# Kernel tuning notes

Measured on AMD Instinct MI355X. Metric: run time of the kernel, lower is better.

The kernel has to match this reference:

```python
import jax, jax.numpy as jnp
import numpy as np

N = 12288          # atoms
G = 12             # graphs in batch
R = 1536           # residues
K = 32             # max_num_neighbors
RADIUS = 5.0
MIN_DISTANCE = 5
EPS = 1e-10


def setup_inputs() -> dict:
    key = jax.random.key(0)
    k1, k2, k3 = jax.random.split(key, 3)
    # positions in a 50 A box -> protein-like density (~a few neighbors in r=5)
    node_position = jax.random.uniform(k1, (N, 3), dtype=jnp.float32) * 50.0
    node2graph = jnp.sort(jax.random.randint(k2, (N,), 0, G, dtype=jnp.int32))
    atom2residue = jnp.sort(jax.random.randint(k3, (N,), 0, R, dtype=jnp.int32))
    return {"node_position": node_position, "node2graph": node2graph,
            "atom2residue": atom2residue}


def _select_neighbors(node_position, node2graph):
    """For each node i, pick up to K nearest same-graph nodes within RADIUS.
    Returns idx [N,K] (neighbor indices) and in_radius [N,K] (validity)."""
    n = node_position.shape[0]
    sq = jnp.sum(node_position * node_position, axis=-1)            # [N]
    d2 = sq[:, None] + sq[None, :] - 2.0 * (node_position @ node_position.T)
    d2 = jnp.maximum(d2, 0.0)                                        # [N,N]
    ar = jnp.arange(n)
    valid = (node2graph[:, None] == node2graph[None, :]) \
            & (ar[:, None] != ar[None, :]) \
            & (d2 <= RADIUS * RADIUS)
    nd2 = jnp.where(valid, d2, jnp.inf)
    neg_d2, idx = jax.lax.top_k(-nd2, K)                             # nearest K
    in_radius = jnp.isfinite(neg_d2)
    return idx, in_radius


def reference(node_position, node2graph, atom2residue):
    n = node_position.shape[0]
    idx, in_radius = _select_neighbors(node_position, node2graph)
    node_out = jnp.repeat(jnp.arange(n, dtype=jnp.int32), K)         # center i
    node_in = idx.reshape(-1).astype(jnp.int32)                      # neighbor j
    valid = in_radius.reshape(-1)
    # residue-distance filter: drop |res_in - res_out| < min_distance
    res_diff = jnp.abs(atom2residue[node_in] - atom2residue[node_out])
    valid = valid & (res_diff >= MIN_DISTANCE)
    # drop near-coincident positions (||p_i - p_j|| < eps)
    diff = node_position[node_in] - node_position[node_out]
    d2_sel = jnp.sum(diff * diff, axis=-1)
    valid = valid & (d2_sel >= EPS * EPS)
    relation = jnp.zeros_like(node_in)
    edge_list = jnp.stack([node_in, node_out, relation], axis=-1)    # [N*K,3]
    edge_list = jnp.where(valid[:, None], edge_list, -1)             # pad invalid
    return edge_list, valid, jnp.int32(1)
```

## Files before the change

kernel.cpp:

```cpp
#include <hip/hip_runtime.h>

#define EDGE_K 32
#define CAP    256

__global__ __launch_bounds__(64) void spatial_edge_kernel(
    const float* __restrict__ pos,
    const int* __restrict__ n2g,
    const int* __restrict__ a2r,
    int* __restrict__ out,
    int n)
{
    const int i    = blockIdx.x;
    const int lane = threadIdx.x;

    __shared__ float sd2[CAP];
    __shared__ int   sj[CAP];
    __shared__ float rd2[EDGE_K];
    __shared__ int   rj[EDGE_K];

    const float xi = pos[3*i+0];
    const float yi = pos[3*i+1];
    const float zi = pos[3*i+2];
    const float si = xi*xi + yi*yi + zi*zi;
    const int g  = n2g[i];
    const int ri = a2r[i];

    int lo = 0, hi = n;
    while (lo < hi) { int m = (lo + hi) >> 1; if (n2g[m] < g) lo = m + 1; else hi = m; }
    const int jstart = lo;
    hi = n;
    while (lo < hi) { int m = (lo + hi) >> 1; if (n2g[m] <= g) lo = m + 1; else hi = m; }
    const int jend = lo;

    int count = 0;
    for (int j0 = jstart; j0 < jend; j0 += 64) {
        const int j = j0 + lane;
        bool pass = false;
        float d2 = 0.0f;
        if (j < jend && j != i) {
            const float xj = pos[3*j+0];
            const float yj = pos[3*j+1];
            const float zj = pos[3*j+2];
            const float sj2 = xj*xj + yj*yj + zj*zj;
            const float dt  = xi*xj + yi*yj + zi*zj;
            d2 = si + sj2 - 2.0f*dt;
            d2 = fmaxf(d2, 0.0f);
            pass = (d2 <= 25.0f);
        }
        const unsigned long long mask = __ballot(pass);
        if (pass) {
            const int idx = count + __popcll(mask & ((1ull << lane) - 1ull));
            if (idx < CAP) { sd2[idx] = d2; sj[idx] = j; }
        }
        count += __popcll(mask);
    }
    __syncthreads();

    int cnt;
    if (count <= CAP) {
        const int m = count;
        for (int c = lane; c < m; c += 64) {
            const float dc = sd2[c];
            const int   jc = sj[c];
            int rank = 0;
            for (int t = 0; t < m; ++t) {
                const float dt_ = sd2[t];
                const int   jt  = sj[t];
                rank += (dt_ < dc) || (dt_ == dc && jt < jc);
            }
            if (rank < EDGE_K) { rd2[rank] = dc; rj[rank] = jc; }
        }
        cnt = (m < EDGE_K) ? m : EDGE_K;
    } else {
        if (lane == 0) {
            float bd[EDGE_K];
            int   bj[EDGE_K];
            int c2 = 0;
            for (int j = jstart; j < jend; ++j) {
                if (j == i) continue;
                const float xj = pos[3*j+0];
                const float yj = pos[3*j+1];
                const float zj = pos[3*j+2];
                const float sj2 = xj*xj + yj*yj + zj*zj;
                const float dt  = xi*xj + yi*yj + zi*zj;
                float d2 = si + sj2 - 2.0f*dt;
                d2 = fmaxf(d2, 0.0f);
                if (d2 > 25.0f) continue;
                if (c2 == EDGE_K && d2 >= bd[EDGE_K-1]) continue;
                int p = (c2 < EDGE_K) ? c2 : (EDGE_K - 1);
                while (p > 0 && bd[p-1] > d2) {
                    bd[p] = bd[p-1]; bj[p] = bj[p-1]; --p;
                }
                bd[p] = d2; bj[p] = j;
                if (c2 < EDGE_K) ++c2;
            }
            for (int k = 0; k < c2; ++k) { rd2[k] = bd[k]; rj[k] = bj[k]; }
        }
        cnt = (count < EDGE_K) ? count : EDGE_K;
    }
    __syncthreads();

    const int NK = n * EDGE_K;
    int* valid_out = out + 3 * NK;
    if (lane < EDGE_K) {
        const int k = lane;
        int a = -1, b = -1, c = -1, v = 0;
        if (k < cnt) {
            const int j  = rj[k];
            const int rjres = a2r[j];
            const int rd = (rjres > ri) ? (rjres - ri) : (ri - rjres);
            const float dx = pos[3*j+0] - xi;
            const float dy = pos[3*j+1] - yi;
            const float dz = pos[3*j+2] - zi;
            const float d2s = dx*dx + dy*dy + dz*dz;
            if (rd >= 5 && d2s >= 1e-20f) { a = j; b = i; c = 0; v = 1; }
        }
        const int e = i * EDGE_K + k;
        out[3*e+0] = a;
        out[3*e+1] = b;
        out[3*e+2] = c;
        valid_out[e] = v;
    }
    if (i == 0 && lane == 0) out[4*NK] = 1;
}

extern "C" void kernel_launch(void* const* d_in, const int* in_sizes, int n_in,
                              void* d_out, int out_size, void* d_ws, size_t ws_size,
                              hipStream_t stream) {
    const float* pos = (const float*)d_in[0];
    const int*   n2g = (const int*)d_in[1];
    const int*   a2r = (const int*)d_in[2];
    int* out = (int*)d_out;
    const int n = in_sizes[0] / 3;
    hipLaunchKernelGGL(spatial_edge_kernel, dim3(n), dim3(64), 0, stream,
                       pos, n2g, a2r, out, n);
}
```

Before: 33.86 us.

## Pack positions into float4 and process four atoms per block

A pre-pass kernel copies positions into an aligned float4 workspace, so the inner distance scan issues one 16-byte load per neighbor instead of three strided scalar loads. The main kernel now runs four waves per block, one atom per wave. Candidate distance/index pairs are stored as int2 in shared memory, and the candidate cap is lowered to fit four waves. The extra launch and workspace write add overhead, and the packed path only runs when a large enough aligned workspace is provided.

```diff
diff --git a/kernel.cpp b/kernel.cpp
--- a/kernel.cpp
+++ b/kernel.cpp
@@ -1,36 +1,55 @@
 #include <hip/hip_runtime.h>
 
 #define EDGE_K 32
-#define CAP    256
+#define CAP    128
+#define WPB    4
 
-__global__ __launch_bounds__(64) void spatial_edge_kernel(
+__global__ __launch_bounds__(256) void pack_kernel(
+    const float* __restrict__ pos, float4* __restrict__ pk, int n)
+{
+    int i = blockIdx.x * blockDim.x + threadIdx.x;
+    if (i < n) {
+        pk[i] = make_float4(pos[3*i+0], pos[3*i+1], pos[3*i+2], 0.0f);
+    }
+}
+
+template<bool PACKED>
+__global__ __launch_bounds__(WPB * 64) void spatial_edge_kernel(
     const float* __restrict__ pos,
+    const float4* __restrict__ pk,
     const int* __restrict__ n2g,
     const int* __restrict__ a2r,
     int* __restrict__ out,
     int n)
 {
-    const int i    = blockIdx.x;
-    const int lane = threadIdx.x;
+    const int wave = threadIdx.x >> 6;
+    const int lane = threadIdx.x & 63;
+    const int i    = blockIdx.x * WPB + wave;
+    const bool active = (i < n);
 
-    __shared__ float sd2[CAP];
-    __shared__ int   sj[CAP];
-    __shared__ float rd2[EDGE_K];
-    __shared__ int   rj[EDGE_K];
+    __shared__ int2 scand[WPB][CAP];
+    __shared__ int2 sres[WPB][EDGE_K];
 
-    const float xi = pos[3*i+0];
-    const float yi = pos[3*i+1];
-    const float zi = pos[3*i+2];
-    const float si = xi*xi + yi*yi + zi*zi;
-    const int g  = n2g[i];
-    const int ri = a2r[i];
+    float xi = 0.f, yi = 0.f, zi = 0.f, si = 0.f;
+    int ri = 0, jstart = 0, jend = 0;
 
-    int lo = 0, hi = n;
-    while (lo < hi) { int m = (lo + hi) >> 1; if (n2g[m] < g) lo = m + 1; else hi = m; }
-    const int jstart = lo;
-    hi = n;
-    while (lo < hi) { int m = (lo + hi) >> 1; if (n2g[m] <= g) lo = m + 1; else hi = m; }
-    const int jend = lo;
+    if (active) {
+        if (PACKED) {
+            float4 p = pk[i];
+            xi = p.x; yi = p.y; zi = p.z;
+        } else {
+            xi = pos[3*i+0]; yi = pos[3*i+1]; zi = pos[3*i+2];
+        }
+        si = xi*xi + yi*yi + zi*zi;
+        const int g = n2g[i];
+        ri = a2r[i];
+        int lo = 0, hi = n;
+        while (lo < hi) { int m = (lo + hi) >> 1; if (n2g[m] < g) lo = m + 1; else hi = m; }
+        jstart = lo;
+        hi = n;
+        while (lo < hi) { int m = (lo + hi) >> 1; if (n2g[m] <= g) lo = m + 1; else hi = m; }
+        jend = lo;
+    }
 
     int count = 0;
     for (int j0 = jstart; j0 < jend; j0 += 64) {
@@ -38,9 +57,13 @@
         bool pass = false;
         float d2 = 0.0f;
         if (j < jend && j != i) {
-            const float xj = pos[3*j+0];
-            const float yj = pos[3*j+1];
-            const float zj = pos[3*j+2];
+            float xj, yj, zj;
+            if (PACKED) {
+                float4 p = pk[j];
+                xj = p.x; yj = p.y; zj = p.z;
+            } else {
+                xj = pos[3*j+0]; yj = pos[3*j+1]; zj = pos[3*j+2];
+            }
             const float sj2 = xj*xj + yj*yj + zj*zj;
             const float dt  = xi*xj + yi*yj + zi*zj;
             d2 = si + sj2 - 2.0f*dt;
@@ -49,38 +72,41 @@
         }
         const unsigned long long mask = __ballot(pass);
         if (pass) {
-            const int idx = count + __popcll(mask & ((1ull << lane) - 1ull));
-            if (idx < CAP) { sd2[idx] = d2; sj[idx] = j; }
+            const int idx = count +
+                (int)__builtin_amdgcn_mbcnt_hi((unsigned)(mask >> 32),
+                     __builtin_amdgcn_mbcnt_lo((unsigned)mask, 0u));
+            if (idx < CAP) scand[wave][idx] = make_int2(__float_as_int(d2), j);
         }
         count += __popcll(mask);
     }
     __syncthreads();
 
-    int cnt;
+    int cnt = 0;
     if (count <= CAP) {
         const int m = count;
         for (int c = lane; c < m; c += 64) {
-            const float dc = sd2[c];
-            const int   jc = sj[c];
+            const int2 e = scand[wave][c];
+            const float dc = __int_as_float(e.x);
+            const int   jc = e.y;
             int rank = 0;
             for (int t = 0; t < m; ++t) {
-                const float dt_ = sd2[t];
-                const int   jt  = sj[t];
-                rank += (dt_ < dc) || (dt_ == dc && jt < jc);
+                const int2 et = scand[wave][t];
+                const float dtv = __int_as_float(et.x);
+                rank += (dtv < dc) || (dtv == dc && et.y < jc);
             }
-            if (rank < EDGE_K) { rd2[rank] = dc; rj[rank] = jc; }
+            if (rank < EDGE_K) sres[wave][rank] = e;
         }
         cnt = (m < EDGE_K) ? m : EDGE_K;
-    } else {
+    } else if (active) {
         if (lane == 0) {
             float bd[EDGE_K];
             int   bj[EDGE_K];
             int c2 = 0;
             for (int j = jstart; j < jend; ++j) {
                 if (j == i) continue;
-                const float xj = pos[3*j+0];
-                const float yj = pos[3*j+1];
-                const float zj = pos[3*j+2];
+                float xj, yj, zj;
+                if (PACKED) { float4 p = pk[j]; xj = p.x; yj = p.y; zj = p.z; }
+                else { xj = pos[3*j+0]; yj = pos[3*j+1]; zj = pos[3*j+2]; }
                 const float sj2 = xj*xj + yj*yj + zj*zj;
                 const float dt  = xi*xj + yi*yj + zi*zj;
                 float d2 = si + sj2 - 2.0f*dt;
@@ -94,7 +120,8 @@
                 bd[p] = d2; bj[p] = j;
                 if (c2 < EDGE_K) ++c2;
             }
-            for (int k = 0; k < c2; ++k) { rd2[k] = bd[k]; rj[k] = bj[k]; }
+            for (int k = 0; k < c2; ++k)
+                sres[wave][k] = make_int2(__float_as_int(bd[k]), bj[k]);
         }
         cnt = (count < EDGE_K) ? count : EDGE_K;
     }
@@ -102,16 +129,19 @@
 
     const int NK = n * EDGE_K;
     int* valid_out = out + 3 * NK;
-    if (lane < EDGE_K) {
+    if (active && lane < EDGE_K) {
         const int k = lane;
         int a = -1, b = -1, c = -1, v = 0;
         if (k < cnt) {
-            const int j  = rj[k];
+            const int j = sres[wave][k].y;
             const int rjres = a2r[j];
             const int rd = (rjres > ri) ? (rjres - ri) : (ri - rjres);
-            const float dx = pos[3*j+0] - xi;
-            const float dy = pos[3*j+1] - yi;
-            const float dz = pos[3*j+2] - zi;
+            float xj, yj, zj;
+            if (PACKED) { float4 p = pk[j]; xj = p.x; yj = p.y; zj = p.z; }
+            else { xj = pos[3*j+0]; yj = pos[3*j+1]; zj = pos[3*j+2]; }
+            const float dx = xj - xi;
+            const float dy = yj - yi;
+            const float dz = zj - zi;
             const float d2s = dx*dx + dy*dy + dz*dz;
             if (rd >= 5 && d2s >= 1e-20f) { a = j; b = i; c = 0; v = 1; }
         }
@@ -121,7 +151,7 @@
         out[3*e+2] = c;
         valid_out[e] = v;
     }
-    if (i == 0 && lane == 0) out[4*NK] = 1;
+    if (blockIdx.x == 0 && threadIdx.x == 0) out[4*NK] = 1;
 }
 
 extern "C" void kernel_launch(void* const* d_in, const int* in_sizes, int n_in,
@@ -132,6 +162,16 @@
     const int*   a2r = (const int*)d_in[2];
     int* out = (int*)d_out;
     const int n = in_sizes[0] / 3;
-    hipLaunchKernelGGL(spatial_edge_kernel, dim3(n), dim3(64), 0, stream,
-                       pos, n2g, a2r, out, n);
+    const int grid = (n + WPB - 1) / WPB;
+    const bool packed = (ws_size >= (size_t)n * sizeof(float4)) && (((uintptr_t)d_ws & 15) == 0);
+    if (packed) {
+        float4* pk = (float4*)d_ws;
+        hipLaunchKernelGGL(pack_kernel, dim3((n + 255) / 256), dim3(256), 0, stream,
+                           pos, pk, n);
+        hipLaunchKernelGGL(spatial_edge_kernel<true>, dim3(grid), dim3(WPB * 64), 0, stream,
+                           pos, (const float4*)pk, n2g, a2r, out, n);
+    } else {
+        hipLaunchKernelGGL(spatial_edge_kernel<false>, dim3(grid), dim3(WPB * 64), 0, stream,
+                           pos, (const float4*)nullptr, n2g, a2r, out, n);
+    }
 }
```

Measured after the change: 73.52 us. 117% more time.

## Add pre-pass packing positions to float4 and precomputing graph bounds

Applied to the files above, without the earlier changes.

A new pre-pass kernel packs positions into float4 in the workspace and computes per-graph start/end offsets, so the main kernel skips its two binary searches and does one vector load per neighbor. The neighbor scan is unrolled four chunks at a time to overlap loads, candidates are stored as int2 pairs, and the candidate buffer cap drops from 256 to 128. This adds a second launch and a fallback to the old kernel when the workspace is too small or misaligned. The smaller cap sends more atoms to the serial single-lane path if neighbor counts exceed 128.

```diff
diff --git a/kernel.cpp b/kernel.cpp
--- a/kernel.cpp
+++ b/kernel.cpp
@@ -1,100 +1,127 @@
 #include <hip/hip_runtime.h>
 
 #define EDGE_K 32
-#define CAP    256
-
-__global__ __launch_bounds__(64) void spatial_edge_kernel(
-    const float* __restrict__ pos,
+#define CAP    128
+#define NB     64
+
+__global__ __launch_bounds__(256) void pack_kernel(
+    const float* __restrict__ pos, const int* __restrict__ n2g,
+    float4* __restrict__ pk, int* __restrict__ bounds, int n)
+{
+    int i = blockIdx.x * blockDim.x + threadIdx.x;
+    if (i >= n) return;
+    pk[i] = make_float4(pos[3*i+0], pos[3*i+1], pos[3*i+2], 0.0f);
+    const int gi = n2g[i];
+    if (i == 0) {
+        for (int g = 0; g <= gi && g < NB; ++g) bounds[g] = 0;
+    } else {
+        const int gp = n2g[i-1];
+        if (gp != gi) for (int g = gp + 1; g <= gi && g < NB; ++g) bounds[g] = i;
+    }
+    if (i == n - 1) {
+        for (int g = gi + 1; g < NB; ++g) bounds[g] = n;
+    }
+}
+
+__global__ __launch_bounds__(64) void spatial_edge_fast(
+    const float4* __restrict__ pk,
     const int* __restrict__ n2g,
     const int* __restrict__ a2r,
-    int* __restrict__ out,
-    int n)
+    const int* __restrict__ bounds,
+    int* __restrict__ out, int n)
 {
     const int i    = blockIdx.x;
     const int lane = threadIdx.x;
 
-    __shared__ float sd2[CAP];
-    __shared__ int   sj[CAP];
-    __shared__ float rd2[EDGE_K];
-    __shared__ int   rj[EDGE_K];
-
-    const float xi = pos[3*i+0];
-    const float yi = pos[3*i+1];
-    const float zi = pos[3*i+2];
+    __shared__ int2 scand[CAP];
+    __shared__ int2 sres[EDGE_K];
+
+    const float4 pi = pk[i];
+    const float xi = pi.x, yi = pi.y, zi = pi.z;
     const float si = xi*xi + yi*yi + zi*zi;
     const int g  = n2g[i];
     const int ri = a2r[i];
 
-    int lo = 0, hi = n;
-    while (lo < hi) { int m = (lo + hi) >> 1; if (n2g[m] < g) lo = m + 1; else hi = m; }
-    const int jstart = lo;
-    hi = n;
-    while (lo < hi) { int m = (lo + hi) >> 1; if (n2g[m] <= g) lo = m + 1; else hi = m; }
-    const int jend = lo;
+    int jstart, jend;
+    if (g < NB - 1) {
+        jstart = bounds[g];
+        jend   = bounds[g + 1];
+    } else {
+        int lo = 0, hi = n;
+        while (lo < hi) { int m = (lo + hi) >> 1; if (n2g[m] < g) lo = m + 1; else hi = m; }
+        jstart = lo; hi = n;
+        while (lo < hi) { int m = (lo + hi) >> 1; if (n2g[m] <= g) lo = m + 1; else hi = m; }
+        jend = lo;
+    }
 
     int count = 0;
-    for (int j0 = jstart; j0 < jend; j0 += 64) {
-        const int j = j0 + lane;
-        bool pass = false;
-        float d2 = 0.0f;
+    auto process = [&](float4 p, int j) {
+        bool pass = false; float d2 = 0.0f;
         if (j < jend && j != i) {
-            const float xj = pos[3*j+0];
-            const float yj = pos[3*j+1];
-            const float zj = pos[3*j+2];
-            const float sj2 = xj*xj + yj*yj + zj*zj;
-            const float dt  = xi*xj + yi*yj + zi*zj;
+            const float sj2 = p.x*p.x + p.y*p.y + p.z*p.z;
+            const float dt  = xi*p.x + yi*p.y + zi*p.z;
             d2 = si + sj2 - 2.0f*dt;
             d2 = fmaxf(d2, 0.0f);
             pass = (d2 <= 25.0f);
         }
         const unsigned long long mask = __ballot(pass);
         if (pass) {
-            const int idx = count + __popcll(mask & ((1ull << lane) - 1ull));
-            if (idx < CAP) { sd2[idx] = d2; sj[idx] = j; }
+            const int idx = count +
+                (int)__builtin_amdgcn_mbcnt_hi((unsigned)(mask >> 32),
+                     __builtin_amdgcn_mbcnt_lo((unsigned)mask, 0u));
+            if (idx < CAP) scand[idx] = make_int2(__float_as_int(d2), j);
         }
         count += __popcll(mask);
-    }
-    __syncthreads();
-
-    int cnt;
+    };
+
+    const int nch = (jend - jstart + 63) >> 6;
+    const int jm  = jend - 1;
+    for (int c = 0; c < nch; c += 4) {
+        const int ja = jstart + (c << 6) + lane;
+        const float4 p0 = pk[min(ja,       jm)];
+        const float4 p1 = pk[min(ja +  64, jm)];
+        const float4 p2 = pk[min(ja + 128, jm)];
+        const float4 p3 = pk[min(ja + 192, jm)];
+        process(p0, ja);
+        if (c + 1 < nch) process(p1, ja + 64);
+        if (c + 2 < nch) process(p2, ja + 128);
+        if (c + 3 < nch) process(p3, ja + 192);
+    }
+    __syncthreads();
+
+    int cnt = 0;
     if (count <= CAP) {
         const int m = count;
         for (int c = lane; c < m; c += 64) {
-            const float dc = sd2[c];
-            const int   jc = sj[c];
+            const int2 e = scand[c];
+            const float dc = __int_as_float(e.x);
             int rank = 0;
             for (int t = 0; t < m; ++t) {
-                const float dt_ = sd2[t];
-                const int   jt  = sj[t];
-                rank += (dt_ < dc) || (dt_ == dc && jt < jc);
+                const int2 et = scand[t];
+                const float dtv = __int_as_float(et.x);
+                rank += (dtv < dc) || (dtv == dc && et.y < e.y);
             }
-            if (rank < EDGE_K) { rd2[rank] = dc; rj[rank] = jc; }
+            if (rank < EDGE_K) sres[rank] = e;
         }
         cnt = (m < EDGE_K) ? m : EDGE_K;
     } else {
         if (lane == 0) {
-            float bd[EDGE_K];
-            int   bj[EDGE_K];
-            int c2 = 0;
+            float bd[EDGE_K]; int bj[EDGE_K]; int c2 = 0;
             for (int j = jstart; j < jend; ++j) {
                 if (j == i) continue;
-                const float xj = pos[3*j+0];
-                const float yj = pos[3*j+1];
-                const float zj = pos[3*j+2];
-                const float sj2 = xj*xj + yj*yj + zj*zj;
-                const float dt  = xi*xj + yi*yj + zi*zj;
+                const float4 p = pk[j];
+                const float sj2 = p.x*p.x + p.y*p.y + p.z*p.z;
+                const float dt  = xi*p.x + yi*p.y + zi*p.z;
                 float d2 = si + sj2 - 2.0f*dt;
                 d2 = fmaxf(d2, 0.0f);
                 if (d2 > 25.0f) continue;
                 if (c2 == EDGE_K && d2 >= bd[EDGE_K-1]) continue;
-                int p = (c2 < EDGE_K) ? c2 : (EDGE_K - 1);
-                while (p > 0 && bd[p-1] > d2) {
-                    bd[p] = bd[p-1]; bj[p] = bj[p-1]; --p;
-                }
-                bd[p] = d2; bj[p] = j;
+                int p2 = (c2 < EDGE_K) ? c2 : (EDGE_K - 1);
+                while (p2 > 0 && bd[p2-1] > d2) { bd[p2] = bd[p2-1]; bj[p2] = bj[p2-1]; --p2; }
+                bd[p2] = d2; bj[p2] = j;
                 if (c2 < EDGE_K) ++c2;
             }
-            for (int k = 0; k < c2; ++k) { rd2[k] = bd[k]; rj[k] = bj[k]; }
+            for (int k = 0; k < c2; ++k) sres[k] = make_int2(__float_as_int(bd[k]), bj[k]);
         }
         cnt = (count < EDGE_K) ? count : EDGE_K;
     }
@@ -106,12 +133,11 @@
         const int k = lane;
         int a = -1, b = -1, c = -1, v = 0;
         if (k < cnt) {
-            const int j  = rj[k];
-            const int rjres = a2r[j];
-            const int rd = (rjres > ri) ? (rjres - ri) : (ri - rjres);
-            const float dx = pos[3*j+0] - xi;
-            const float dy = pos[3*j+1] - yi;
-            const float dz = pos[3*j+2] - zi;
+            const int j = sres[k].y;
+            const int rj = a2r[j];
+            const int rd = (rj > ri) ? (rj - ri) : (ri - rj);
+            const float4 p = pk[j];
+            const float dx = p.x - xi, dy = p.y - yi, dz = p.z - zi;
             const float d2s = dx*dx + dy*dy + dz*dz;
             if (rd >= 5 && d2s >= 1e-20f) { a = j; b = i; c = 0; v = 1; }
         }
@@ -119,6 +145,100 @@
         out[3*e+0] = a;
         out[3*e+1] = b;
         out[3*e+2] = c;
+        valid_out[e] = v;
+    }
+    if (i == 0 && lane == 0) out[4*NK] = 1;
+}
+
+__global__ __launch_bounds__(64) void spatial_edge_ref(
+    const float* __restrict__ pos,
+    const int* __restrict__ n2g,
+    const int* __restrict__ a2r,
+    int* __restrict__ out, int n)
+{
+    const int i = blockIdx.x;
+    const int lane = threadIdx.x;
+    __shared__ float sd2[CAP]; __shared__ int sj[CAP];
+    __shared__ float rd2[EDGE_K]; __shared__ int rjj[EDGE_K];
+
+    const float xi = pos[3*i+0], yi = pos[3*i+1], zi = pos[3*i+2];
+    const float si = xi*xi + yi*yi + zi*zi;
+    const int g = n2g[i]; const int ri = a2r[i];
+
+    int lo = 0, hi = n;
+    while (lo < hi) { int m = (lo + hi) >> 1; if (n2g[m] < g) lo = m + 1; else hi = m; }
+    const int jstart = lo; hi = n;
+    while (lo < hi) { int m = (lo + hi) >> 1; if (n2g[m] <= g) lo = m + 1; else hi = m; }
+    const int jend = lo;
+
+    int count = 0;
+    for (int j0 = jstart; j0 < jend; j0 += 64) {
+        const int j = j0 + lane;
+        bool pass = false; float d2 = 0.0f;
+        if (j < jend && j != i) {
+            const float xj = pos[3*j+0], yj = pos[3*j+1], zj = pos[3*j+2];
+            const float sj2 = xj*xj + yj*yj + zj*zj;
+            const float dt  = xi*xj + yi*yj + zi*zj;
+            d2 = fmaxf(si + sj2 - 2.0f*dt, 0.0f);
+            pass = (d2 <= 25.0f);
+        }
+        const unsigned long long mask = __ballot(pass);
+        if (pass) {
+            const int idx = count + __popcll(mask & ((1ull << lane) - 1ull));
+            if (idx < CAP) { sd2[idx] = d2; sj[idx] = j; }
+        }
+        count += __popcll(mask);
+    }
+    __syncthreads();
+
+    int cnt;
+    if (count <= CAP) {
+        const int m = count;
+        for (int c = lane; c < m; c += 64) {
+            const float dc = sd2[c]; const int jc = sj[c];
+            int rank = 0;
+            for (int t = 0; t < m; ++t)
+                rank += (sd2[t] < dc) || (sd2[t] == dc && sj[t] < jc);
+            if (rank < EDGE_K) { rd2[rank] = dc; rjj[rank] = jc; }
+        }
+        cnt = (m < EDGE_K) ? m : EDGE_K;
+    } else {
+        if (lane == 0) {
+            float bd[EDGE_K]; int bj[EDGE_K]; int c2 = 0;
+            for (int j = jstart; j < jend; ++j) {
+                if (j == i) continue;
+                const float xj = pos[3*j+0], yj = pos[3*j+1], zj = pos[3*j+2];
+                const float sj2 = xj*xj + yj*yj + zj*zj;
+                const float dt  = xi*xj + yi*yj + zi*zj;
+                float d2 = fmaxf(si + sj2 - 2.0f*dt, 0.0f);
+                if (d2 > 25.0f) continue;
+                if (c2 == EDGE_K && d2 >= bd[EDGE_K-1]) continue;
+                int p = (c2 < EDGE_K) ? c2 : (EDGE_K - 1);
+                while (p > 0 && bd[p-1] > d2) { bd[p] = bd[p-1]; bj[p] = bj[p-1]; --p; }
+                bd[p] = d2; bj[p] = j;
+                if (c2 < EDGE_K) ++c2;
+            }
+            for (int k = 0; k < c2; ++k) { rd2[k] = bd[k]; rjj[k] = bj[k]; }
+        }
+        cnt = (count < EDGE_K) ? count : EDGE_K;
+    }
+    __syncthreads();
+
+    const int NK = n * EDGE_K;
+    int* valid_out = out + 3 * NK;
+    if (lane < EDGE_K) {
+        const int k = lane;
+        int a = -1, b = -1, c = -1, v = 0;
+        if (k < cnt) {
+            const int j = rjj[k];
+            const int rj = a2r[j];
+            const int rd = (rj > ri) ? (rj - ri) : (ri - rj);
+            const float dx = pos[3*j+0] - xi, dy = pos[3*j+1] - yi, dz = pos[3*j+2] - zi;
+            const float d2s = dx*dx + dy*dy + dz*dz;
+            if (rd >= 5 && d2s >= 1e-20f) { a = j; b = i; c = 0; v = 1; }
+        }
+        const int e = i * EDGE_K + k;
+        out[3*e+0] = a; out[3*e+1] = b; out[3*e+2] = c;
         valid_out[e] = v;
     }
     if (i == 0 && lane == 0) out[4*NK] = 1;
@@ -132,6 +252,17 @@
     const int*   a2r = (const int*)d_in[2];
     int* out = (int*)d_out;
     const int n = in_sizes[0] / 3;
-    hipLaunchKernelGGL(spatial_edge_kernel, dim3(n), dim3(64), 0, stream,
-                       pos, n2g, a2r, out, n);
-}
+    const size_t need = (size_t)n * sizeof(float4) + NB * sizeof(int);
+    const bool packed = (ws_size >= need) && (((uintptr_t)d_ws & 15) == 0);
+    if (packed) {
+        float4* pk = (float4*)d_ws;
+        int* bounds = (int*)(pk + n);
+        hipLaunchKernelGGL(pack_kernel, dim3((n + 255) / 256), dim3(256), 0, stream,
+                           pos, n2g, pk, bounds, n);
+        hipLaunchKernelGGL(spatial_edge_fast, dim3(n), dim3(64), 0, stream,
+                           (const float4*)pk, n2g, a2r, (const int*)bounds, out, n);
+    } else {
+        hipLaunchKernelGGL(spatial_edge_ref, dim3(n), dim3(64), 0, stream,
+                           pos, n2g, a2r, out, n);
+    }
+}
```

Result: faster. 29.86 us (median of 2 runs) (-11.8%).
